# Performance work log

Measured on AMD Instinct MI355X. Metric: run time of the kernel, lower is better.

## Reference

```python
import jax, jax.numpy as jnp
import numpy as np

N_NODES = 50000


def sage_conv(x, edge_index, w_l, w_r, b):
    # PyG SAGEConv (aggr='mean', root_weight=True):
    #   out = mean_{j in N(i)} x_j @ w_l + x_i @ w_r + b
    src = edge_index[0]  # message source j
    dst = edge_index[1]  # message target i
    msgs = x[src]                                        # [E, C_in] gather
    agg = jax.ops.segment_sum(msgs, dst, num_segments=N_NODES)   # [N, C_in]
    deg = jax.ops.segment_sum(jnp.ones((src.shape[0],), x.dtype), dst,
                              num_segments=N_NODES)              # [N]
    agg = agg / jnp.maximum(deg, 1.0)[:, None]           # mean aggregation
    return agg @ w_l + x @ w_r + b


def setup_inputs() -> dict:
    key = jax.random.key(0)
    ks = jax.random.split(key, 8)
    in_c, hid_c, out_c = 96, 128, 64
    x = jax.random.normal(ks[0], (N_NODES, in_c), dtype=jnp.float32)
    edge_index = jax.random.randint(ks[1], (2, 800000), 0, N_NODES, dtype=jnp.int64)
    def glorot(k, fan_in, fan_out):
        lim = float(np.sqrt(6.0 / (fan_in + fan_out)))
        return jax.random.uniform(k, (fan_in, fan_out), jnp.float32, -lim, lim)
    return {
        'x': x,
        'edge_index': edge_index,
        'w1_l': glorot(ks[2], in_c, hid_c),
        'w1_r': glorot(ks[3], in_c, hid_c),
        'b1': jnp.zeros((hid_c,), jnp.float32),
        'w2_l': glorot(ks[4], hid_c, out_c),
        'w2_r': glorot(ks[5], hid_c, out_c),
        'b2': jnp.zeros((out_c,), jnp.float32),
    }


def reference(x, edge_index, w1_l, w1_r, b1, w2_l, w2_r, b2):
    h = sage_conv(x, edge_index, w1_l, w1_r, b1)
    h = jax.nn.relu(h)
    out = sage_conv(h, edge_index, w2_l, w2_r, b2)
    return out
```

## Files before the change

### kernel.cpp

```cpp
#include <hip/hip_runtime.h>
#include <hip/hip_bf16.h>

#define N_NODES 50000
#define IN_C    96
#define HID_C   128
#define OUT_C   64
#define MROWS   50048

#define NB      200
#define BSZ     250
#define WCHUNK  4096
#define NWG     196
#define BCAP    8192

#define XBLKS   2344
#define WBLKS   160

typedef __attribute__((ext_vector_type(8))) short short8;
typedef __attribute__((ext_vector_type(4))) float f32x4;

__device__ inline unsigned int f2bf(float f) {
    unsigned int u = __float_as_uint(f);
    return (u + 0x7fffu + ((u >> 16) & 1u)) >> 16;
}
__device__ inline unsigned int pack2(float lo, float hi) {
    return f2bf(lo) | (f2bf(hi) << 16);
}
__device__ inline float blo(unsigned int u) { return __uint_as_float(u << 16); }
__device__ inline float bhi(unsigned int u) { return __uint_as_float(u & 0xffff0000u); }

__global__ __launch_bounds__(256) void conv_all_kernel(
    const float* __restrict__ x, uint4* __restrict__ xb4,
    const float* __restrict__ w1l, const float* __restrict__ w1r,
    const float* __restrict__ w2l, const float* __restrict__ w2r,
    unsigned short* __restrict__ wt1, unsigned short* __restrict__ wt2,
    int* __restrict__ gcnt)
{
    int blk = blockIdx.x;
    if (blk == gridDim.x - 1 && threadIdx.x < NB) gcnt[threadIdx.x] = 0;
    if (blk < XBLKS) {
        int idx = blk * 256 + threadIdx.x;
        if (idx >= N_NODES * 12) return;
        const float4* x4 = (const float4*)x;
        float4 u = x4[(size_t)idx * 2];
        float4 v = x4[(size_t)idx * 2 + 1];
        uint4 w;
        w.x = pack2(u.x, u.y); w.y = pack2(u.z, u.w);
        w.z = pack2(v.x, v.y); w.w = pack2(v.z, v.w);
        xb4[idx] = w;
    } else {
        int i = (blk - XBLKS) * 256 + threadIdx.x;
        if (i < 128 * 192) {
            int col = i / 192, k = i - col * 192;
            float v = (k < 96) ? w1l[k * 128 + col] : w1r[(k - 96) * 128 + col];
            wt1[i] = (unsigned short)f2bf(v);
        } else {
            int j = i - 128 * 192;
            int col = j / 128, k = j - col * 128;
            float v = (col < 64) ? w2l[k * 64 + col] : w2r[k * 64 + col - 64];
            wt2[j] = (unsigned short)f2bf(v);
        }
    }
}

__global__ __launch_bounds__(256) void csr_scatter(
    const int* __restrict__ src, const int* __restrict__ dst,
    int* __restrict__ gcnt, unsigned int* __restrict__ pairs, int E)
{
    __shared__ int lsrc[WCHUNK];
    __shared__ int ldst[WCHUNK];
    __shared__ int h[NB];
    __shared__ int wbase[NB];
    int t = threadIdx.x;
    int base_e = blockIdx.x * WCHUNK;
    int rem = E - base_e; if (rem > WCHUNK) rem = WCHUNK;
    {
        const int4* s4 = (const int4*)(src + base_e);
        const int4* d4 = (const int4*)(dst + base_e);
        int nv = rem >> 2;
        for (int k = t; k < nv; k += 256) {
            ((int4*)lsrc)[k] = s4[k];
            ((int4*)ldst)[k] = d4[k];
        }
        for (int i = (nv << 2) + t; i < rem; i += 256) {
            lsrc[i] = src[base_e + i];
            ldst[i] = dst[base_e + i];
        }
    }
    if (t < NB) h[t] = 0;
    __syncthreads();
    for (int i = t; i < rem; i += 256)
        atomicAdd(&h[ldst[i] / BSZ], 1);
    __syncthreads();
    if (t < NB) {
        wbase[t] = atomicAdd(&gcnt[t], h[t]);
        h[t] = 0;
    }
    __syncthreads();
    for (int i = t; i < rem; i += 256) {
        int d = ldst[i];
        int b = d / BSZ;
        int r = atomicAdd(&h[b], 1);
        pairs[b * BCAP + wbase[b] + r] =
            ((unsigned)(d - b * BSZ) << 17) | (unsigned)lsrc[i];
    }
}

__global__ __launch_bounds__(256) void partb_csr(
    const unsigned int* __restrict__ pairs, const int* __restrict__ gcnt,
    int* __restrict__ rowstart, int* __restrict__ cnt,
    int* __restrict__ adj)
{
    __shared__ int h[256];
    __shared__ int buf[256];
    __shared__ int cur[256];
    int b = blockIdx.x;
    int t = threadIdx.x;
    int beg = b * BCAP;
    int n = gcnt[b];
    int node0 = b * BSZ;
    h[t] = 0;
    __syncthreads();
    const uint4* p4 = (const uint4*)(pairs + beg);
    int nv = n >> 2;
    for (int k = t; k < nv; k += 256) {
        uint4 u = p4[k];
        atomicAdd(&h[u.x >> 17], 1);
        atomicAdd(&h[u.y >> 17], 1);
        atomicAdd(&h[u.z >> 17], 1);
        atomicAdd(&h[u.w >> 17], 1);
    }
    for (int i = (nv << 2) + t; i < n; i += 256)
        atomicAdd(&h[pairs[beg + i] >> 17], 1);
    __syncthreads();
    int c = h[t];
    buf[t] = c;
    __syncthreads();
    for (int off = 1; off < 256; off <<= 1) {
        int v = (t >= off) ? buf[t - off] : 0;
        __syncthreads();
        buf[t] += v;
        __syncthreads();
    }
    int excl = buf[t] - c;
    if (t < BSZ) {
        rowstart[node0 + t] = beg + excl;
        cnt[node0 + t] = c;
    }
    cur[t] = beg + excl;
    __syncthreads();
    for (int k = t; k < nv; k += 256) {
        uint4 u = p4[k];
        int p0 = atomicAdd(&cur[u.x >> 17], 1);
        int p1 = atomicAdd(&cur[u.y >> 17], 1);
        int p2 = atomicAdd(&cur[u.z >> 17], 1);
        int p3 = atomicAdd(&cur[u.w >> 17], 1);
        adj[p0] = (int)(u.x & 0x1FFFFu);
        adj[p1] = (int)(u.y & 0x1FFFFu);
        adj[p2] = (int)(u.z & 0x1FFFFu);
        adj[p3] = (int)(u.w & 0x1FFFFu);
    }
    for (int i = (nv << 2) + t; i < n; i += 256) {
        unsigned int u = pairs[beg + i];
        int pos = atomicAdd(&cur[u >> 17], 1);
        adj[pos] = (int)(u & 0x1FFFFu);
    }
}

__global__ __launch_bounds__(256) void gather1_kernel(
    const int* __restrict__ rowstart, const int* __restrict__ cnt,
    const int* __restrict__ adj, const uint4* __restrict__ xb4,
    uint4* __restrict__ agg4)
{
    int idx = blockIdx.x * 256 + threadIdx.x;
    if (idx >= N_NODES * 12) return;
    int node = idx / 12;
    int c = idx - node * 12;
    int beg = rowstart[node];
    int d = cnt[node];
    int end = beg + d;
    float a0=0,a1=0,a2=0,a3=0,a4=0,a5=0,a6=0,a7=0;
    float b0=0,b1=0,b2=0,b3=0,b4=0,b5=0,b6=0,b7=0;
    int j = beg;
    for (; j + 3 < end; j += 4) {
        int s0 = adj[j];
        int s1 = adj[j + 1];
        int s2 = adj[j + 2];
        int s3 = adj[j + 3];
        uint4 u = xb4[(size_t)s0 * 12 + c];
        uint4 v = xb4[(size_t)s1 * 12 + c];
        uint4 w = xb4[(size_t)s2 * 12 + c];
        uint4 z = xb4[(size_t)s3 * 12 + c];
        a0 += blo(u.x); a1 += bhi(u.x); a2 += blo(u.y); a3 += bhi(u.y);
        a4 += blo(u.z); a5 += bhi(u.z); a6 += blo(u.w); a7 += bhi(u.w);
        b0 += blo(v.x); b1 += bhi(v.x); b2 += blo(v.y); b3 += bhi(v.y);
        b4 += blo(v.z); b5 += bhi(v.z); b6 += blo(v.w); b7 += bhi(v.w);
        a0 += blo(w.x); a1 += bhi(w.x); a2 += blo(w.y); a3 += bhi(w.y);
        a4 += blo(w.z); a5 += bhi(w.z); a6 += blo(w.w); a7 += bhi(w.w);
        b0 += blo(z.x); b1 += bhi(z.x); b2 += blo(z.y); b3 += bhi(z.y);
        b4 += blo(z.z); b5 += bhi(z.z); b6 += blo(z.w); b7 += bhi(z.w);
    }
    for (; j < end; j++) {
        int s0 = adj[j];
        uint4 u = xb4[(size_t)s0 * 12 + c];
        a0 += blo(u.x); a1 += bhi(u.x); a2 += blo(u.y); a3 += bhi(u.y);
        a4 += blo(u.z); a5 += bhi(u.z); a6 += blo(u.w); a7 += bhi(u.w);
    }
    a0 += b0; a1 += b1; a2 += b2; a3 += b3;
    a4 += b4; a5 += b5; a6 += b6; a7 += b7;
    float id = 1.0f / (float)max(d, 1);
    uint4 w;
    w.x = pack2(a0 * id, a1 * id); w.y = pack2(a2 * id, a3 * id);
    w.z = pack2(a4 * id, a5 * id); w.w = pack2(a6 * id, a7 * id);
    agg4[(size_t)node * 12 + c] = w;
}

__global__ __launch_bounds__(256) void gemm12_fused(
    const uint4* __restrict__ agg4, const uint4* __restrict__ xb4,
    const uint4* __restrict__ w1t4, const uint4* __restrict__ w2t4,
    const float* __restrict__ b1, const float* __restrict__ b2,
    unsigned short* __restrict__ p, float* __restrict__ out)
{
    constexpr int KP = 200;
    constexpr int KQ = 136;
    __shared__ unsigned short lw[128 * KP];
    __shared__ unsigned short la[64 * KP];
    int t = threadIdx.x;
    uint4* lw4 = (uint4*)lw;
    uint4* la4 = (uint4*)la;

    for (int i = t; i < 128 * 24; i += 256) {
        int r = i / 24, c = i - r * 24;
        lw4[r * 25 + c] = w1t4[i];
    }
    int row0 = blockIdx.x * 64;
    for (int i = t; i < 64 * 24; i += 256) {
        int r = i / 24, c = i - r * 24;
        la4[r * 25 + c] = (c < 12)
            ? agg4[(size_t)(row0 + r) * 12 + c]
            : xb4[(size_t)(row0 + r) * 12 + (c - 12)];
    }
    __syncthreads();

    int wave = t >> 6, lane = t & 63;
    int m = lane & 15, half = lane >> 4;
    int koff = half * 8;
    f32x4 acc[4][2] = {};
#pragma unroll
    for (int k0 = 0; k0 < 192; k0 += 32) {
        short8 B0 = *(const short8*)&lw[(wave * 32 + m)      * KP + k0 + koff];
        short8 B1 = *(const short8*)&lw[(wave * 32 + 16 + m) * KP + k0 + koff];
#pragma unroll
        for (int g = 0; g < 4; g++) {
            short8 A = *(const short8*)&la[(g * 16 + m) * KP + k0 + koff];
            acc[g][0] = __builtin_amdgcn_mfma_f32_16x16x32_bf16(A, B0, acc[g][0], 0, 0, 0);
            acc[g][1] = __builtin_amdgcn_mfma_f32_16x16x32_bf16(A, B1, acc[g][1], 0, 0, 0);
        }
    }
    __syncthreads();

    int col0 = wave * 32 + m, col1 = col0 + 16;
    {
        float bias0 = b1[col0], bias1 = b1[col1];
#pragma unroll
        for (int g = 0; g < 4; g++) {
#pragma unroll
            for (int reg = 0; reg < 4; reg++) {
                int hr = g * 16 + half * 4 + reg;
                la[hr * KQ + col0] = (unsigned short)f2bf(fmaxf(acc[g][0][reg] + bias0, 0.f));
                la[hr * KQ + col1] = (unsigned short)f2bf(fmaxf(acc[g][1][reg] + bias1, 0.f));
            }
        }
    }
    for (int i = t; i < 128 * 16; i += 256) {
        int r = i >> 4, c = i & 15;
        lw4[r * 17 + c] = w2t4[i];
    }
    __syncthreads();

    f32x4 acc2[4][2] = {};
#pragma unroll
    for (int k0 = 0; k0 < 128; k0 += 32) {
        short8 B0 = *(const short8*)&lw[(wave * 32 + m)      * KQ + k0 + koff];
        short8 B1 = *(const short8*)&lw[(wave * 32 + 16 + m) * KQ + k0 + koff];
#pragma unroll
        for (int g = 0; g < 4; g++) {
            short8 A = *(const short8*)&la[(g * 16 + m) * KQ + k0 + koff];
            acc2[g][0] = __builtin_amdgcn_mfma_f32_16x16x32_bf16(A, B0, acc2[g][0], 0, 0, 0);
            acc2[g][1] = __builtin_amdgcn_mfma_f32_16x16x32_bf16(A, B1, acc2[g][1], 0, 0, 0);
        }
    }
#pragma unroll
    for (int g = 0; g < 4; g++) {
#pragma unroll
        for (int reg = 0; reg < 4; reg++) {
            int r = row0 + g * 16 + half * 4 + reg;
            if (r >= N_NODES) continue;
            float v0 = acc2[g][0][reg], v1 = acc2[g][1][reg];
            if (col0 < 64) p[(size_t)r * 64 + col0] = (unsigned short)f2bf(v0);
            else           out[(size_t)r * 64 + col0 - 64] = v0 + b2[col0 - 64];
            if (col1 < 64) p[(size_t)r * 64 + col1] = (unsigned short)f2bf(v1);
            else           out[(size_t)r * 64 + col1 - 64] = v1 + b2[col1 - 64];
        }
    }
}

__global__ __launch_bounds__(256) void gather2_kernel(
    const int* __restrict__ rowstart, const int* __restrict__ cnt,
    const int* __restrict__ adj, const uint4* __restrict__ p4,
    float* __restrict__ out)
{
    int idx = blockIdx.x * 256 + threadIdx.x;
    if (idx >= N_NODES * 8) return;
    int node = idx >> 3;
    int c = idx & 7;
    int beg = rowstart[node];
    int d = cnt[node];
    int end = beg + d;
    float a0=0,a1=0,a2=0,a3=0,a4=0,a5=0,a6=0,a7=0;
    float b0=0,b1=0,b2=0,b3=0,b4=0,b5=0,b6=0,b7=0;
    int j = beg;
    for (; j + 3 < end; j += 4) {
        int s0 = adj[j];
        int s1 = adj[j + 1];
        int s2 = adj[j + 2];
        int s3 = adj[j + 3];
        uint4 u = p4[(size_t)s0 * 8 + c];
        uint4 v = p4[(size_t)s1 * 8 + c];
        uint4 w = p4[(size_t)s2 * 8 + c];
        uint4 z = p4[(size_t)s3 * 8 + c];
        a0 += blo(u.x); a1 += bhi(u.x); a2 += blo(u.y); a3 += bhi(u.y);
        a4 += blo(u.z); a5 += bhi(u.z); a6 += blo(u.w); a7 += bhi(u.w);
        b0 += blo(v.x); b1 += bhi(v.x); b2 += blo(v.y); b3 += bhi(v.y);
        b4 += blo(v.z); b5 += bhi(v.z); b6 += blo(v.w); b7 += bhi(v.w);
        a0 += blo(w.x); a1 += bhi(w.x); a2 += blo(w.y); a3 += bhi(w.y);
        a4 += blo(w.z); a5 += bhi(w.z); a6 += blo(w.w); a7 += bhi(w.w);
        b0 += blo(z.x); b1 += bhi(z.x); b2 += blo(z.y); b3 += bhi(z.y);
        b4 += blo(z.z); b5 += bhi(z.z); b6 += blo(z.w); b7 += bhi(z.w);
    }
    for (; j < end; j++) {
        int s0 = adj[j];
        uint4 u = p4[(size_t)s0 * 8 + c];
        a0 += blo(u.x); a1 += bhi(u.x); a2 += blo(u.y); a3 += bhi(u.y);
        a4 += blo(u.z); a5 += bhi(u.z); a6 += blo(u.w); a7 += bhi(u.w);
    }
    a0 += b0; a1 += b1; a2 += b2; a3 += b3;
    a4 += b4; a5 += b5; a6 += b6; a7 += b7;
    float id = 1.0f / (float)max(d, 1);
    float4* o4 = (float4*)out;
    size_t base = (size_t)node * 16 + 2 * c;
    float4 u = o4[base], v = o4[base + 1];
    u.x = fmaf(a0, id, u.x); u.y = fmaf(a1, id, u.y);
    u.z = fmaf(a2, id, u.z); u.w = fmaf(a3, id, u.w);
    v.x = fmaf(a4, id, v.x); v.y = fmaf(a5, id, v.y);
    v.z = fmaf(a6, id, v.z); v.w = fmaf(a7, id, v.w);
    o4[base] = u; o4[base + 1] = v;
}

extern "C" void kernel_launch(void* const* d_in, const int* in_sizes, int n_in,
                              void* d_out, int out_size, void* d_ws, size_t ws_size,
                              hipStream_t stream)
{
    const float* x   = (const float*)d_in[0];
    const int*   ei  = (const int*)d_in[1];
    const float* w1l = (const float*)d_in[2];
    const float* w1r = (const float*)d_in[3];
    const float* b1  = (const float*)d_in[4];
    const float* w2l = (const float*)d_in[5];
    const float* w2r = (const float*)d_in[6];
    const float* b2  = (const float*)d_in[7];
    float* out = (float*)d_out;

    int E = in_sizes[1] / 2;
    const int* src = ei;
    const int* dst = ei + E;

    int* gcnt     = (int*)d_ws;
    int* cnt      = gcnt + 256;
    int* rowstart = cnt + N_NODES;
    unsigned int* pairs = (unsigned int*)(rowstart + N_NODES);
    int* adj      = (int*)(pairs + NB * BCAP);
    unsigned short* xb  = (unsigned short*)(adj + NB * BCAP);
    unsigned short* agg = xb + (size_t)MROWS * IN_C;
    unsigned short* p   = agg + (size_t)MROWS * IN_C;
    unsigned short* Wt1 = p  + (size_t)N_NODES * 64;
    unsigned short* Wt2 = Wt1 + 128 * 192;

    conv_all_kernel<<<XBLKS + WBLKS, 256, 0, stream>>>(
        x, (uint4*)xb, w1l, w1r, w2l, w2r, Wt1, Wt2, gcnt);

    csr_scatter<<<NWG, 256, 0, stream>>>(src, dst, gcnt, pairs, E);
    partb_csr<<<NB, 256, 0, stream>>>(pairs, gcnt, rowstart, cnt, adj);

    gather1_kernel<<<(N_NODES * 12 + 255) / 256, 256, 0, stream>>>(
        rowstart, cnt, adj, (const uint4*)xb, (uint4*)agg);

    gemm12_fused<<<MROWS / 64, 256, 0, stream>>>(
        (const uint4*)agg, (const uint4*)xb, (const uint4*)Wt1, (const uint4*)Wt2,
        b1, b2, p, out);

    gather2_kernel<<<(N_NODES * 8 + 255) / 256, 256, 0, stream>>>(
        rowstart, cnt, adj, (const uint4*)p, out);
}
```

Before: 170.4 us.

## Fuse edge scatter with conversion kernel, halve bucket size, unroll gathers by eight

Merges the CSR edge-scatter kernel and the bf16 conversion kernel into one launch, so the scatter blocks run alongside the x/weight conversion blocks. A memset now zeroes the global bucket counters, since the scatter can no longer rely on an earlier kernel to do it. Bucket count doubles to 400 with 125 nodes per bucket, giving more partb_csr blocks with less work each. The gather loops are unrolled to eight neighbours to put more loads in flight. The trade-off is that every block of the merged kernel reserves 32KB of shared memory, which may lower occupancy for the conversion blocks.

```diff
diff --git a/kernel.cpp b/kernel.cpp
--- a/kernel.cpp
+++ b/kernel.cpp
@@ -7,11 +7,11 @@
 #define OUT_C   64
 #define MROWS   50048
 
-#define NB      200
-#define BSZ     250
+#define NB      400
+#define BSZ     125
 #define WCHUNK  4096
 #define NWG     196
-#define BCAP    8192
+#define BCAP    4096
 
 #define XBLKS   2344
 #define WBLKS   160
@@ -29,17 +29,58 @@
 __device__ inline float blo(unsigned int u) { return __uint_as_float(u << 16); }
 __device__ inline float bhi(unsigned int u) { return __uint_as_float(u & 0xffff0000u); }
 
-__global__ __launch_bounds__(256) void conv_all_kernel(
+__global__ __launch_bounds__(256) void scatter_conv_kernel(
+    const int* __restrict__ src, const int* __restrict__ dst,
+    int* __restrict__ gcnt, unsigned int* __restrict__ pairs, int E,
     const float* __restrict__ x, uint4* __restrict__ xb4,
     const float* __restrict__ w1l, const float* __restrict__ w1r,
     const float* __restrict__ w2l, const float* __restrict__ w2r,
-    unsigned short* __restrict__ wt1, unsigned short* __restrict__ wt2,
-    int* __restrict__ gcnt)
-{
+    unsigned short* __restrict__ wt1, unsigned short* __restrict__ wt2)
+{
+    __shared__ int lsrc[WCHUNK];
+    __shared__ int ldst[WCHUNK];
+    __shared__ int h[NB];
+    __shared__ int wbase[NB];
     int blk = blockIdx.x;
-    if (blk == gridDim.x - 1 && threadIdx.x < NB) gcnt[threadIdx.x] = 0;
+    int t = threadIdx.x;
+    if (blk < NWG) {
+        int base_e = blk * WCHUNK;
+        int rem = E - base_e; if (rem > WCHUNK) rem = WCHUNK;
+        {
+            const int4* s4 = (const int4*)(src + base_e);
+            const int4* d4 = (const int4*)(dst + base_e);
+            int nv = rem >> 2;
+            for (int k = t; k < nv; k += 256) {
+                ((int4*)lsrc)[k] = s4[k];
+                ((int4*)ldst)[k] = d4[k];
+            }
+            for (int i = (nv << 2) + t; i < rem; i += 256) {
+                lsrc[i] = src[base_e + i];
+                ldst[i] = dst[base_e + i];
+            }
+        }
+        for (int i = t; i < NB; i += 256) h[i] = 0;
+        __syncthreads();
+        for (int i = t; i < rem; i += 256)
+            atomicAdd(&h[ldst[i] / BSZ], 1);
+        __syncthreads();
+        for (int i = t; i < NB; i += 256) {
+            wbase[i] = atomicAdd(&gcnt[i], h[i]);
+            h[i] = 0;
+        }
+        __syncthreads();
+        for (int i = t; i < rem; i += 256) {
+            int d = ldst[i];
+            int b = d / BSZ;
+            int r = atomicAdd(&h[b], 1);
+            pairs[b * BCAP + wbase[b] + r] =
+                ((unsigned)(d - b * BSZ) << 17) | (unsigned)lsrc[i];
+        }
+        return;
+    }
+    blk -= NWG;
     if (blk < XBLKS) {
-        int idx = blk * 256 + threadIdx.x;
+        int idx = blk * 256 + t;
         if (idx >= N_NODES * 12) return;
         const float4* x4 = (const float4*)x;
         float4 u = x4[(size_t)idx * 2];
@@ -49,7 +90,7 @@
         w.z = pack2(v.x, v.y); w.w = pack2(v.z, v.w);
         xb4[idx] = w;
     } else {
-        int i = (blk - XBLKS) * 256 + threadIdx.x;
+        int i = (blk - XBLKS) * 256 + t;
         if (i < 128 * 192) {
             int col = i / 192, k = i - col * 192;
             float v = (k < 96) ? w1l[k * 128 + col] : w1r[(k - 96) * 128 + col];
@@ -60,49 +101,6 @@
             float v = (col < 64) ? w2l[k * 64 + col] : w2r[k * 64 + col - 64];
             wt2[j] = (unsigned short)f2bf(v);
         }
-    }
-}
-
-__global__ __launch_bounds__(256) void csr_scatter(
-    const int* __restrict__ src, const int* __restrict__ dst,
-    int* __restrict__ gcnt, unsigned int* __restrict__ pairs, int E)
-{
-    __shared__ int lsrc[WCHUNK];
-    __shared__ int ldst[WCHUNK];
-    __shared__ int h[NB];
-    __shared__ int wbase[NB];
-    int t = threadIdx.x;
-    int base_e = blockIdx.x * WCHUNK;
-    int rem = E - base_e; if (rem > WCHUNK) rem = WCHUNK;
-    {
-        const int4* s4 = (const int4*)(src + base_e);
-        const int4* d4 = (const int4*)(dst + base_e);
-        int nv = rem >> 2;
-        for (int k = t; k < nv; k += 256) {
-            ((int4*)lsrc)[k] = s4[k];
-            ((int4*)ldst)[k] = d4[k];
-        }
-        for (int i = (nv << 2) + t; i < rem; i += 256) {
-            lsrc[i] = src[base_e + i];
-            ldst[i] = dst[base_e + i];
-        }
-    }
-    if (t < NB) h[t] = 0;
-    __syncthreads();
-    for (int i = t; i < rem; i += 256)
-        atomicAdd(&h[ldst[i] / BSZ], 1);
-    __syncthreads();
-    if (t < NB) {
-        wbase[t] = atomicAdd(&gcnt[t], h[t]);
-        h[t] = 0;
-    }
-    __syncthreads();
-    for (int i = t; i < rem; i += 256) {
-        int d = ldst[i];
-        int b = d / BSZ;
-        int r = atomicAdd(&h[b], 1);
-        pairs[b * BCAP + wbase[b] + r] =
-            ((unsigned)(d - b * BSZ) << 17) | (unsigned)lsrc[i];
     }
 }
 
@@ -167,6 +165,13 @@
     }
 }
 
+#define ACC8(u) do { \
+    a0 += blo(u.x); a1 += bhi(u.x); a2 += blo(u.y); a3 += bhi(u.y); \
+    a4 += blo(u.z); a5 += bhi(u.z); a6 += blo(u.w); a7 += bhi(u.w); } while (0)
+#define BCC8(u) do { \
+    b0 += blo(u.x); b1 += bhi(u.x); b2 += blo(u.y); b3 += bhi(u.y); \
+    b4 += blo(u.z); b5 += bhi(u.z); b6 += blo(u.w); b7 += bhi(u.w); } while (0)
+
 __global__ __launch_bounds__(256) void gather1_kernel(
     const int* __restrict__ rowstart, const int* __restrict__ cnt,
     const int* __restrict__ adj, const uint4* __restrict__ xb4,
@@ -182,29 +187,34 @@
     float a0=0,a1=0,a2=0,a3=0,a4=0,a5=0,a6=0,a7=0;
     float b0=0,b1=0,b2=0,b3=0,b4=0,b5=0,b6=0,b7=0;
     int j = beg;
+    for (; j + 7 < end; j += 8) {
+        int s0 = adj[j];     int s1 = adj[j + 1];
+        int s2 = adj[j + 2]; int s3 = adj[j + 3];
+        int s4 = adj[j + 4]; int s5 = adj[j + 5];
+        int s6 = adj[j + 6]; int s7 = adj[j + 7];
+        uint4 u0 = xb4[(size_t)s0 * 12 + c];
+        uint4 u1 = xb4[(size_t)s1 * 12 + c];
+        uint4 u2 = xb4[(size_t)s2 * 12 + c];
+        uint4 u3 = xb4[(size_t)s3 * 12 + c];
+        uint4 u4 = xb4[(size_t)s4 * 12 + c];
+        uint4 u5 = xb4[(size_t)s5 * 12 + c];
+        uint4 u6 = xb4[(size_t)s6 * 12 + c];
+        uint4 u7 = xb4[(size_t)s7 * 12 + c];
+        ACC8(u0); BCC8(u1); ACC8(u2); BCC8(u3);
+        ACC8(u4); BCC8(u5); ACC8(u6); BCC8(u7);
+    }
     for (; j + 3 < end; j += 4) {
-        int s0 = adj[j];
-        int s1 = adj[j + 1];
-        int s2 = adj[j + 2];
-        int s3 = adj[j + 3];
-        uint4 u = xb4[(size_t)s0 * 12 + c];
-        uint4 v = xb4[(size_t)s1 * 12 + c];
-        uint4 w = xb4[(size_t)s2 * 12 + c];
-        uint4 z = xb4[(size_t)s3 * 12 + c];
-        a0 += blo(u.x); a1 += bhi(u.x); a2 += blo(u.y); a3 += bhi(u.y);
-        a4 += blo(u.z); a5 += bhi(u.z); a6 += blo(u.w); a7 += bhi(u.w);
-        b0 += blo(v.x); b1 += bhi(v.x); b2 += blo(v.y); b3 += bhi(v.y);
-        b4 += blo(v.z); b5 += bhi(v.z); b6 += blo(v.w); b7 += bhi(v.w);
-        a0 += blo(w.x); a1 += bhi(w.x); a2 += blo(w.y); a3 += bhi(w.y);
-        a4 += blo(w.z); a5 += bhi(w.z); a6 += blo(w.w); a7 += bhi(w.w);
-        b0 += blo(z.x); b1 += bhi(z.x); b2 += blo(z.y); b3 += bhi(z.y);
-        b4 += blo(z.z); b5 += bhi(z.z); b6 += blo(z.w); b7 += bhi(z.w);
+        int s0 = adj[j];     int s1 = adj[j + 1];
+        int s2 = adj[j + 2]; int s3 = adj[j + 3];
+        uint4 u0 = xb4[(size_t)s0 * 12 + c];
+        uint4 u1 = xb4[(size_t)s1 * 12 + c];
+        uint4 u2 = xb4[(size_t)s2 * 12 + c];
+        uint4 u3 = xb4[(size_t)s3 * 12 + c];
+        ACC8(u0); BCC8(u1); ACC8(u2); BCC8(u3);
     }
     for (; j < end; j++) {
-        int s0 = adj[j];
-        uint4 u = xb4[(size_t)s0 * 12 + c];
-        a0 += blo(u.x); a1 += bhi(u.x); a2 += blo(u.y); a3 += bhi(u.y);
-        a4 += blo(u.z); a5 += bhi(u.z); a6 += blo(u.w); a7 += bhi(u.w);
+        uint4 u = xb4[(size_t)adj[j] * 12 + c];
+        ACC8(u);
     }
     a0 += b0; a1 += b1; a2 += b2; a3 += b3;
     a4 += b4; a5 += b5; a6 += b6; a7 += b7;
@@ -320,29 +330,34 @@
     float a0=0,a1=0,a2=0,a3=0,a4=0,a5=0,a6=0,a7=0;
     float b0=0,b1=0,b2=0,b3=0,b4=0,b5=0,b6=0,b7=0;
     int j = beg;
+    for (; j + 7 < end; j += 8) {
+        int s0 = adj[j];     int s1 = adj[j + 1];
+        int s2 = adj[j + 2]; int s3 = adj[j + 3];
+        int s4 = adj[j + 4]; int s5 = adj[j + 5];
+        int s6 = adj[j + 6]; int s7 = adj[j + 7];
+        uint4 u0 = p4[(size_t)s0 * 8 + c];
+        uint4 u1 = p4[(size_t)s1 * 8 + c];
+        uint4 u2 = p4[(size_t)s2 * 8 + c];
+        uint4 u3 = p4[(size_t)s3 * 8 + c];
+        uint4 u4 = p4[(size_t)s4 * 8 + c];
+        uint4 u5 = p4[(size_t)s5 * 8 + c];
+        uint4 u6 = p4[(size_t)s6 * 8 + c];
+        uint4 u7 = p4[(size_t)s7 * 8 + c];
+        ACC8(u0); BCC8(u1); ACC8(u2); BCC8(u3);
+        ACC8(u4); BCC8(u5); ACC8(u6); BCC8(u7);
+    }
     for (; j + 3 < end; j += 4) {
-        int s0 = adj[j];
-        int s1 = adj[j + 1];
-        int s2 = adj[j + 2];
-        int s3 = adj[j + 3];
-        uint4 u = p4[(size_t)s0 * 8 + c];
-        uint4 v = p4[(size_t)s1 * 8 + c];
-        uint4 w = p4[(size_t)s2 * 8 + c];
-        uint4 z = p4[(size_t)s3 * 8 + c];
-        a0 += blo(u.x); a1 += bhi(u.x); a2 += blo(u.y); a3 += bhi(u.y);
-        a4 += blo(u.z); a5 += bhi(u.z); a6 += blo(u.w); a7 += bhi(u.w);
-        b0 += blo(v.x); b1 += bhi(v.x); b2 += blo(v.y); b3 += bhi(v.y);
-        b4 += blo(v.z); b5 += bhi(v.z); b6 += blo(v.w); b7 += bhi(v.w);
-        a0 += blo(w.x); a1 += bhi(w.x); a2 += blo(w.y); a3 += bhi(w.y);
-        a4 += blo(w.z); a5 += bhi(w.z); a6 += blo(w.w); a7 += bhi(w.w);
-        b0 += blo(z.x); b1 += bhi(z.x); b2 += blo(z.y); b3 += bhi(z.y);
-        b4 += blo(z.z); b5 += bhi(z.z); b6 += blo(z.w); b7 += bhi(z.w);
+        int s0 = adj[j];     int s1 = adj[j + 1];
+        int s2 = adj[j + 2]; int s3 = adj[j + 3];
+        uint4 u0 = p4[(size_t)s0 * 8 + c];
+        uint4 u1 = p4[(size_t)s1 * 8 + c];
+        uint4 u2 = p4[(size_t)s2 * 8 + c];
+        uint4 u3 = p4[(size_t)s3 * 8 + c];
+        ACC8(u0); BCC8(u1); ACC8(u2); BCC8(u3);
     }
     for (; j < end; j++) {
-        int s0 = adj[j];
-        uint4 u = p4[(size_t)s0 * 8 + c];
-        a0 += blo(u.x); a1 += bhi(u.x); a2 += blo(u.y); a3 += bhi(u.y);
-        a4 += blo(u.z); a5 += bhi(u.z); a6 += blo(u.w); a7 += bhi(u.w);
+        uint4 u = p4[(size_t)adj[j] * 8 + c];
+        ACC8(u);
     }
     a0 += b0; a1 += b1; a2 += b2; a3 += b3;
     a4 += b4; a5 += b5; a6 += b6; a7 += b7;
@@ -376,7 +391,7 @@
     const int* dst = ei + E;
 
     int* gcnt     = (int*)d_ws;
-    int* cnt      = gcnt + 256;
+    int* cnt      = gcnt + 512;
     int* rowstart = cnt + N_NODES;
     unsigned int* pairs = (unsigned int*)(rowstart + N_NODES);
     int* adj      = (int*)(pairs + NB * BCAP);
@@ -386,10 +401,12 @@
     unsigned short* Wt1 = p  + (size_t)N_NODES * 64;
     unsigned short* Wt2 = Wt1 + 128 * 192;
 
-    conv_all_kernel<<<XBLKS + WBLKS, 256, 0, stream>>>(
-        x, (uint4*)xb, w1l, w1r, w2l, w2r, Wt1, Wt2, gcnt);
-
-    csr_scatter<<<NWG, 256, 0, stream>>>(src, dst, gcnt, pairs, E);
+    hipMemsetAsync(gcnt, 0, NB * sizeof(int), stream);
+
+    scatter_conv_kernel<<<NWG + XBLKS + WBLKS, 256, 0, stream>>>(
+        src, dst, gcnt, pairs, E,
+        x, (uint4*)xb, w1l, w1r, w2l, w2r, Wt1, Wt2);
+
     partb_csr<<<NB, 256, 0, stream>>>(pairs, gcnt, rowstart, cnt, adj);
 
     gather1_kernel<<<(N_NODES * 12 + 255) / 256, 256, 0, stream>>>(
```

Result: no change. 172.3 us (+1.1%).
